# Kernel optimization log

Hardware: AMD Instinct MI355X
Metric: run time of the kernel (lower is better)

The kernel has to match this reference:

```python
import jax, jax.numpy as jnp
import numpy as np

N = 100000        # nodes
E = 1_600_000     # edges (avg degree 16)
F_IN = 128        # in_channels
HID = 64          # hidden_channels (per-head)
H1 = 4            # heads layer 1
G = 128           # number of graphs
NEG_SLOPE = 0.2   # PyG GATConv default leaky_relu slope


def setup_inputs() -> dict:
    key = jax.random.key(0)
    ks = jax.random.split(key, 12)
    x = jax.random.normal(ks[0], (N, F_IN), dtype=jnp.float32)
    edge_index = jax.random.randint(ks[1], (2, E), 0, N, dtype=jnp.int64)
    batch = jnp.sort(jax.random.randint(ks[2], (N,), 0, G, dtype=jnp.int64))
    s1 = 1.0 / np.sqrt(F_IN)
    s2 = 1.0 / np.sqrt(H1 * HID)
    # layer 1: in=F_IN, out=H1*HID (PyG lin has no bias; separate bias after concat)
    w1 = jax.random.normal(ks[3], (H1 * HID, F_IN), dtype=jnp.float32) * s1
    a_src1 = jax.random.normal(ks[4], (H1, HID), dtype=jnp.float32) * s1
    a_dst1 = jax.random.normal(ks[5], (H1, HID), dtype=jnp.float32) * s1
    b1 = jnp.zeros((H1 * HID,), dtype=jnp.float32)
    # layer 2: in=H1*HID, out=HID, heads=1
    w2 = jax.random.normal(ks[6], (1 * HID, H1 * HID), dtype=jnp.float32) * s2
    a_src2 = jax.random.normal(ks[7], (1, HID), dtype=jnp.float32) * s2
    a_dst2 = jax.random.normal(ks[8], (1, HID), dtype=jnp.float32) * s2
    b2 = jnp.zeros((HID,), dtype=jnp.float32)
    return {"x": x, "w1": w1, "a_src1": a_src1, "a_dst1": a_dst1, "b1": b1,
            "w2": w2, "a_src2": a_src2, "a_dst2": a_dst2, "b2": b2,
            "edge_index": edge_index, "batch": batch}


def _segment_softmax(alpha, seg, n):
    # numerically-stable softmax of alpha [E,H] grouped by seg (dst node)
    m = jax.ops.segment_max(alpha, seg, num_segments=n)
    m = jnp.where(jnp.isfinite(m), m, 0.0)  # empty segments -> 0
    a = jnp.exp(alpha - m[seg])
    s = jax.ops.segment_sum(a, seg, num_segments=n)
    return a / (s[seg] + 1e-16)


def _gat_conv(x, w, a_src, a_dst, bias, src, dst, n, heads, ch):
    h = (x @ w.T).reshape(n, heads, ch)          # [N,H,C]
    alpha_src = jnp.sum(h * a_src[None], axis=-1)  # [N,H]
    alpha_dst = jnp.sum(h * a_dst[None], axis=-1)  # [N,H]
    e = jax.nn.leaky_relu(alpha_src[src] + alpha_dst[dst], NEG_SLOPE)  # [E,H]
    att = _segment_softmax(e, dst, n)             # [E,H]
    msg = h[src] * att[:, :, None]                # [E,H,C]
    out = jax.ops.segment_sum(msg, dst, num_segments=n)  # [N,H,C]
    return out.reshape(n, heads * ch) + bias


def reference(x, w1, a_src1, a_dst1, b1, w2, a_src2, a_dst2, b2, edge_index, batch):
    src, dst = edge_index[0], edge_index[1]
    h = jax.nn.relu(_gat_conv(x, w1, a_src1, a_dst1, b1, src, dst, N, H1, HID))
    h = jax.nn.relu(_gat_conv(h, w2, a_src2, a_dst2, b2, src, dst, N, 1, HID))
    # global_mean_pool over graph ids
    sums = jax.ops.segment_sum(h, batch, num_segments=G)            # [G,HID]
    cnt = jax.ops.segment_sum(jnp.ones((N,), h.dtype), batch, num_segments=G)
    return sums / jnp.maximum(cnt, 1.0)[:, None]
```

## Files before the change

kernel.cpp:

```cpp
#include <hip/hip_runtime.h>
#include <math.h>
#include <type_traits>

#define NNODES 100000
#define NEDGES 1600000
#define NGRAPH 128
#define NBKT 391
#define CAP 1536
#define EPB 2048

typedef _Float16 f16x4 __attribute__((ext_vector_type(4)));
typedef _Float16 f16x8 __attribute__((ext_vector_type(8)));
typedef float f32x4 __attribute__((ext_vector_type(4)));

__global__ void convert_w(const float* __restrict__ w1, const float* __restrict__ w2,
                          const float* __restrict__ as1c, const float* __restrict__ ad1c,
                          const float* __restrict__ as2c, const float* __restrict__ ad2c,
                          _Float16* __restrict__ w1h, _Float16* __restrict__ w2h,
                          _Float16* __restrict__ va1, _Float16* __restrict__ va2) {
  const int b = blockIdx.x, tid = threadIdx.x;
  if (b < 8) {
    if (tid >= 128) return;
    int h = b & 3;
    const float* coef = (b >= 4) ? ad1c : as1c;
    float s = 0.f;
    for (int c = 0; c < 64; ++c) s = fmaf(w1[(size_t)(h * 64 + c) * 128 + tid], coef[h * 64 + c], s);
    va1[b * 128 + tid] = (_Float16)s;
  } else if (b < 10) {
    int r = b - 8;
    const float* coef = r ? ad2c : as2c;
    float s = 0.f;
    for (int c = 0; c < 64; ++c) s = fmaf(w2[(size_t)c * 256 + tid], coef[c], s);
    va2[r * 256 + tid] = (_Float16)s;
  } else if (b < 138) {
    int i = (b - 10) * 256 + tid;
    w1h[i] = (_Float16)w1[i];
  } else {
    int i = (b - 138) * 256 + tid;
    w2h[i] = (_Float16)w2[i];
  }
}

template <int K, int N, typename AT>
__global__ __launch_bounds__(256) void gemm_mfma(const AT* __restrict__ A,
    const _Float16* __restrict__ Bh, const _Float16* __restrict__ VA,
    _Float16* __restrict__ C, int M, float* __restrict__ asrc, float* __restrict__ adst) {
  constexpr int H = N / 64;
  constexpr int KS = K / 32, NT = N / 16;
  const int lane = threadIdx.x & 63, wid = threadIdx.x >> 6;
  const int lr = lane & 15;
  const int lk = (lane >> 4) * 8;
  const int row = blockIdx.x * 64 + wid * 16 + lr;

  f16x8 a[KS];
  if (row < M) {
    const AT* arow = A + (size_t)row * K;
#pragma unroll
    for (int ks = 0; ks < KS; ++ks) {
      if constexpr (std::is_same<AT, float>::value) {
        float4 v0 = *(const float4*)&arow[ks * 32 + lk];
        float4 v1 = *(const float4*)&arow[ks * 32 + lk + 4];
        f16x8 t;
        t[0] = (_Float16)v0.x; t[1] = (_Float16)v0.y; t[2] = (_Float16)v0.z; t[3] = (_Float16)v0.w;
        t[4] = (_Float16)v1.x; t[5] = (_Float16)v1.y; t[6] = (_Float16)v1.z; t[7] = (_Float16)v1.w;
        a[ks] = t;
      } else {
        a[ks] = *(const f16x8*)&arow[ks * 32 + lk];
      }
    }
  } else {
#pragma unroll
    for (int ks = 0; ks < KS; ++ks) a[ks] = (f16x8){};
  }

  f32x4 accv = (f32x4){0.f, 0.f, 0.f, 0.f};
  {
    const _Float16* vrow = VA + (size_t)lr * K;
#pragma unroll
    for (int ks = 0; ks < KS; ++ks) {
      f16x8 b = *(const f16x8*)&vrow[ks * 32 + lk];
      accv = __builtin_amdgcn_mfma_f32_16x16x32_f16(a[ks], b, accv, 0, 0, 0);
    }
  }

  f32x4 acc[NT];
#pragma unroll
  for (int nt = 0; nt < NT; ++nt) acc[nt] = (f32x4){0.f, 0.f, 0.f, 0.f};
#pragma unroll
  for (int nt = 0; nt < NT; ++nt) {
    const _Float16* brow = Bh + (size_t)(nt * 16 + lr) * K;
#pragma unroll
    for (int ks = 0; ks < KS; ++ks) {
      f16x8 b = *(const f16x8*)&brow[ks * 32 + lk];
      acc[nt] = __builtin_amdgcn_mfma_f32_16x16x32_f16(a[ks], b, acc[nt], 0, 0, 0);
    }
  }

  int row0 = blockIdx.x * 64 + wid * 16 + (lane >> 4) * 4;
#pragma unroll
  for (int r = 0; r < 4; ++r) {
    int orow = row0 + r;
    if (orow >= M) continue;
#pragma unroll
    for (int nt = 0; nt < NT; ++nt)
      C[(size_t)orow * N + nt * 16 + lr] = (_Float16)acc[nt][r];
    if (lr < H) asrc[orow * H + lr] = accv[r];
    else if (lr < 2 * H) adst[orow * H + lr - H] = accv[r];
  }
}

__global__ __launch_bounds__(256) void bucketA(const int* __restrict__ srcv,
    const int* __restrict__ dstv, int2* __restrict__ part, int* __restrict__ gcur,
    int e_count) {
  __shared__ int hist[NBKT];
  __shared__ int base_[NBKT];
  __shared__ int lofs[NBKT];
  const int tid = threadIdx.x;
  const int P = blockIdx.x & 7;
  for (int i = tid; i < NBKT; i += 256) { hist[i] = 0; lofs[i] = 0; }
  __syncthreads();
  const int e0 = blockIdx.x * EPB;
  const int e1 = min(e0 + EPB, e_count);
  for (int e = e0 + tid; e < e1; e += 256) atomicAdd(&hist[dstv[e] >> 8], 1);
  __syncthreads();
  for (int i = tid; i < NBKT; i += 256) {
    int c = hist[i];
    base_[i] = c ? atomicAdd(&gcur[(P * NBKT + i) * 16], c) : 0;
  }
  __syncthreads();
  for (int e = e0 + tid; e < e1; e += 256) {
    int d = dstv[e];
    int b = d >> 8;
    int l = atomicAdd(&lofs[b], 1);
    part[(size_t)(P * NBKT + b) * CAP + base_[b] + l] = make_int2(srcv[e], d);
  }
}

__global__ __launch_bounds__(256) void bucketB1(const int2* __restrict__ part,
    const int* __restrict__ gcur, int* __restrict__ deg, int n) {
  __shared__ int cnt[256];
  const int b = blockIdx.x;
  const int tid = threadIdx.x;
  cnt[tid] = 0;
  __syncthreads();
  for (int P = 0; P < 8; ++P) {
    int cn = gcur[(P * NBKT + b) * 16];
    const int2* seg = part + (size_t)(P * NBKT + b) * CAP;
    for (int i = tid; i < cn; i += 256) atomicAdd(&cnt[seg[i].y & 255], 1);
  }
  __syncthreads();
  int node = (b << 8) + tid;
  if (node < n) deg[node] = cnt[tid];
}

__global__ __launch_bounds__(256) void bucketB2(const int2* __restrict__ part,
    const int* __restrict__ gcur, const int* __restrict__ offsets,
    int* __restrict__ esrc, int n) {
  __shared__ int lcur[256];
  const int b = blockIdx.x;
  const int tid = threadIdx.x;
  int node = (b << 8) + tid;
  lcur[tid] = (node < n) ? offsets[node] : 0;
  __syncthreads();
  for (int P = 0; P < 8; ++P) {
    int cn = gcur[(P * NBKT + b) * 16];
    const int2* seg = part + (size_t)(P * NBKT + b) * CAP;
    for (int i = tid; i < cn; i += 256) {
      int2 e = seg[i];
      int slot = atomicAdd(&lcur[e.y & 255], 1);
      esrc[slot] = e.x;
    }
  }
}

__global__ __launch_bounds__(1024) void scan1(const int* __restrict__ deg, int* __restrict__ inc,
                                              int* __restrict__ bsum, int n) {
  __shared__ int sm[1024];
  int i = blockIdx.x * 1024 + threadIdx.x;
  sm[threadIdx.x] = (i < n) ? deg[i] : 0;
  __syncthreads();
  for (int o = 1; o < 1024; o <<= 1) {
    int t = (threadIdx.x >= o) ? sm[threadIdx.x - o] : 0;
    __syncthreads();
    sm[threadIdx.x] += t;
    __syncthreads();
  }
  if (i < n) inc[i] = sm[threadIdx.x];
  if (threadIdx.x == 1023) bsum[blockIdx.x] = sm[1023];
}

__global__ void scan2(const int* __restrict__ bsum, int* __restrict__ boff, int nb) {
  __shared__ int sm[128];
  int t = threadIdx.x;
  int own = (t < nb) ? bsum[t] : 0;
  sm[t] = own;
  __syncthreads();
  for (int o = 1; o < 128; o <<= 1) {
    int u = (t >= o) ? sm[t - o] : 0;
    __syncthreads();
    sm[t] += u;
    __syncthreads();
  }
  if (t < nb) boff[t] = sm[t] - own;
}

__global__ void scan3(const int* __restrict__ inc, const int* __restrict__ deg,
                      const int* __restrict__ boff, int* __restrict__ offsets,
                      int n, int e_count) {
  int i = blockIdx.x * blockDim.x + threadIdx.x;
  if (i < n) offsets[i] = inc[i] - deg[i] + boff[i >> 10];
  if (i == 0) offsets[n] = e_count;
}

__global__ __launch_bounds__(256) void agg1_kernel(const _Float16* __restrict__ hmat,
    const float* __restrict__ asrc, const float* __restrict__ adst,
    const int* __restrict__ offsets, const int* __restrict__ esrc,
    const float* __restrict__ bias, _Float16* __restrict__ outv) {
  const int lane = threadIdx.x & 63, wid = threadIdx.x >> 6;
  const int node = blockIdx.x * 4 + wid;
  if (node >= NNODES) return;
  const int h = lane >> 4;
  const int start = offsets[node];
  const int end = offsets[node + 1];
  const float adn = adst[node * 4 + h];
  const _Float16* hbase = hmat + lane * 4;
  float acc[4] = {0.f, 0.f, 0.f, 0.f};
  float s = 0.f;
  int j = start;
  for (; j + 8 <= end; j += 8) {
    int sv[8];
#pragma unroll
    for (int t = 0; t < 8; ++t) sv[t] = esrc[j + t];
    f16x4 vv[8];
#pragma unroll
    for (int t = 0; t < 8; ++t) vv[t] = *(const f16x4*)&hbase[(size_t)sv[t] * 256];
    _Float16 ph[8];
#pragma unroll
    for (int t = 0; t < 8; ++t) {
      float v = asrc[sv[t] * 4 + h] + adn;
      v = (v > 0.f) ? v : 0.2f * v;
      float p = __expf(v);
      s += p;
      ph[t] = (_Float16)p;
    }
#pragma unroll
    for (int t = 0; t < 8; ++t)
#pragma unroll
      for (int k = 0; k < 4; ++k)
        acc[k] = fmaf((float)vv[t][k], (float)ph[t], acc[k]);
  }
  for (; j < end; ++j) {
    int sv = esrc[j];
    f16x4 vv = *(const f16x4*)&hbase[(size_t)sv * 256];
    float v = asrc[sv * 4 + h] + adn;
    v = (v > 0.f) ? v : 0.2f * v;
    float p = __expf(v);
    s += p;
    _Float16 phs = (_Float16)p;
#pragma unroll
    for (int k = 0; k < 4; ++k) acc[k] = fmaf((float)vv[k], (float)phs, acc[k]);
  }
  float inv = 1.f / (s + 1e-16f);
  f16x4 ho;
#pragma unroll
  for (int k = 0; k < 4; ++k)
    ho[k] = (_Float16)fmaxf(fmaf(acc[k], inv, bias[lane * 4 + k]), 0.f);
  *(f16x4*)&outv[(size_t)node * 256 + lane * 4] = ho;
}

__global__ __launch_bounds__(256) void agg2_kernel(const _Float16* __restrict__ hmat,
    const float* __restrict__ asrc, const float* __restrict__ adst,
    const int* __restrict__ offsets, const int* __restrict__ esrc,
    const float* __restrict__ bias, float* __restrict__ outv) {
  const int lane = threadIdx.x & 63, wid = threadIdx.x >> 6;
  const int g = lane >> 4, q = lane & 15;
  const int node = blockIdx.x * 16 + wid * 4 + g;
  if (node >= NNODES) return;
  const int start = offsets[node];
  const int end = offsets[node + 1];
  const float adn = adst[node];
  const _Float16* hbase = hmat + q * 4;
  float acc[4] = {0.f, 0.f, 0.f, 0.f};
  float s = 0.f;
  int j = start;
  for (; j + 4 <= end; j += 4) {
    int sv[4];
#pragma unroll
    for (int t = 0; t < 4; ++t) sv[t] = esrc[j + t];
    f16x4 v[4];
#pragma unroll
    for (int t = 0; t < 4; ++t) v[t] = *(const f16x4*)&hbase[(size_t)sv[t] * 64];
#pragma unroll
    for (int t = 0; t < 4; ++t) {
      float x = asrc[sv[t]] + adn;
      x = (x > 0.f) ? x : 0.2f * x;
      float p = __expf(x);
      s += p;
      _Float16 phs = (_Float16)p;
#pragma unroll
      for (int k = 0; k < 4; ++k) acc[k] = fmaf((float)v[t][k], (float)phs, acc[k]);
    }
  }
  for (; j < end; ++j) {
    int sv = esrc[j];
    f16x4 v = *(const f16x4*)&hbase[(size_t)sv * 64];
    float x = asrc[sv] + adn;
    x = (x > 0.f) ? x : 0.2f * x;
    float p = __expf(x);
    s += p;
    _Float16 phs = (_Float16)p;
#pragma unroll
    for (int k = 0; k < 4; ++k) acc[k] = fmaf((float)v[k], (float)phs, acc[k]);
  }
  float inv = 1.f / (s + 1e-16f);
  float4 o;
  o.x = fmaxf(fmaf(acc[0], inv, bias[q * 4 + 0]), 0.f);
  o.y = fmaxf(fmaf(acc[1], inv, bias[q * 4 + 1]), 0.f);
  o.z = fmaxf(fmaf(acc[2], inv, bias[q * 4 + 2]), 0.f);
  o.w = fmaxf(fmaf(acc[3], inv, bias[q * 4 + 3]), 0.f);
  *(float4*)&outv[(size_t)node * 64 + q * 4] = o;
}

__global__ __launch_bounds__(256) void pool_kernel(const float* __restrict__ g2,
    const int* __restrict__ batch, float* __restrict__ out, int n) {
  const int gid = blockIdx.x;
  const int lane = threadIdx.x & 63, w = threadIdx.x >> 6;
  int lo = 0, hi = n;
  while (lo < hi) { int mid = (lo + hi) >> 1; if (batch[mid] < gid) lo = mid + 1; else hi = mid; }
  int lb = lo;
  hi = n;
  while (lo < hi) { int mid = (lo + hi) >> 1; if (batch[mid] < gid + 1) lo = mid + 1; else hi = mid; }
  int ub = lo;
  float acc = 0.f;
  for (int i = lb + w; i < ub; i += 4) acc += g2[(size_t)i * 64 + lane];
  __shared__ float red[4][64];
  red[w][lane] = acc;
  __syncthreads();
  if (threadIdx.x < 64) {
    float sum = (red[0][lane] + red[1][lane]) + (red[2][lane] + red[3][lane]);
    float cnt = fmaxf((float)(ub - lb), 1.f);
    out[gid * 64 + lane] = sum / cnt;
  }
}

extern "C" void kernel_launch(void* const* d_in, const int* in_sizes, int n_in,
                              void* d_out, int out_size, void* d_ws, size_t ws_size,
                              hipStream_t stream) {
  const float* x      = (const float*)d_in[0];
  const float* w1     = (const float*)d_in[1];
  const float* a_src1 = (const float*)d_in[2];
  const float* a_dst1 = (const float*)d_in[3];
  const float* b1     = (const float*)d_in[4];
  const float* w2     = (const float*)d_in[5];
  const float* a_src2 = (const float*)d_in[6];
  const float* a_dst2 = (const float*)d_in[7];
  const float* b2     = (const float*)d_in[8];
  const int*   src    = (const int*)d_in[9];
  const int*   dst    = src + NEDGES;
  const int*   batch  = (const int*)d_in[10];
  float* out = (float*)d_out;

  const int N = NNODES, E = NEDGES;
  const int NB = (N + 1023) / 1024;

  char* wsb = (char*)d_ws;
  size_t off = 0;
  auto alloc = [&](size_t bytes) {
    void* p = wsb + off;
    off = (off + bytes + 255) & ~(size_t)255;
    return p;
  };
  _Float16* h1h = (_Float16*)alloc((size_t)N * 256 * 2);
  _Float16* g1h = (_Float16*)alloc((size_t)N * 256 * 2);
  _Float16* h2h = (_Float16*)alloc((size_t)N * 64 * 2);
  float* g2     = (float*)alloc((size_t)N * 64 * 4);
  float* as1    = (float*)alloc((size_t)N * 4 * 4);
  float* ad1    = (float*)alloc((size_t)N * 4 * 4);
  float* as2    = (float*)alloc((size_t)N * 4);
  float* ad2    = (float*)alloc((size_t)N * 4);
  int* deg      = (int*)alloc((size_t)N * 4);
  int* inc      = (int*)alloc((size_t)N * 4);
  int* bsum     = (int*)alloc((size_t)NB * 4);
  int* boff     = (int*)alloc((size_t)NB * 4);
  int* offsets  = (int*)alloc((size_t)(N + 1) * 4);
  int* esrc     = (int*)alloc((size_t)E * 4);
  int2* part    = (int2*)alloc((size_t)8 * NBKT * CAP * 8);
  int* gcur     = (int*)alloc((size_t)8 * NBKT * 16 * 4);
  _Float16* w1h = (_Float16*)alloc((size_t)256 * 128 * 2);
  _Float16* w2h = (_Float16*)alloc((size_t)64 * 256 * 2);
  _Float16* va1 = (_Float16*)alloc((size_t)16 * 128 * 2);
  _Float16* va2 = (_Float16*)alloc((size_t)16 * 256 * 2);

  hipMemsetAsync(va1, 0, (size_t)16 * 128 * 2, stream);
  hipMemsetAsync(va2, 0, (size_t)16 * 256 * 2, stream);
  convert_w<<<202, 256, 0, stream>>>(w1, w2, a_src1, a_dst1, a_src2, a_dst2,
                                     w1h, w2h, va1, va2);

  hipMemsetAsync(gcur, 0, (size_t)8 * NBKT * 16 * 4, stream);
  bucketA<<<(E + EPB - 1) / EPB, 256, 0, stream>>>(src, dst, part, gcur, E);
  bucketB1<<<NBKT, 256, 0, stream>>>(part, gcur, deg, N);
  scan1<<<NB, 1024, 0, stream>>>(deg, inc, bsum, N);
  scan2<<<1, 128, 0, stream>>>(bsum, boff, NB);
  scan3<<<(N + 255) / 256, 256, 0, stream>>>(inc, deg, boff, offsets, N, E);
  bucketB2<<<NBKT, 256, 0, stream>>>(part, gcur, offsets, esrc, N);

  gemm_mfma<128, 256, float><<<(N + 63) / 64, 256, 0, stream>>>(
      x, w1h, va1, h1h, N, as1, ad1);
  agg1_kernel<<<(N + 3) / 4, 256, 0, stream>>>(h1h, as1, ad1, offsets, esrc, b1, g1h);

  gemm_mfma<256, 64, _Float16><<<(N + 63) / 64, 256, 0, stream>>>(
      g1h, w2h, va2, h2h, N, as2, ad2);
  agg2_kernel<<<(N + 15) / 16, 256, 0, stream>>>(h2h, as2, ad2, offsets, esrc, b2, g2);

  pool_kernel<<<NGRAPH, 256, 0, stream>>>(g2, batch, out, N);
}
```

Before: 411.2 us.

## Prefetch next B tile in MFMA GEMM and split agg1 into four launches

The GEMM now loads all attention-vector B fragments before issuing their MFMAs, and double-buffers the weight fragments, fetching the next N-tile's B rows while the current tile's MFMAs run. This is meant to hide global load latency behind matrix work, at the cost of more registers. Separately, the layer-1 aggregation is split into four sequential launches over node quarters, which adds launch overhead with no obvious benefit. The split looks like an experiment, possibly aimed at cache locality.

```diff
diff --git a/kernel.cpp b/kernel.cpp
--- a/kernel.cpp
+++ b/kernel.cpp
@@ -76,24 +76,36 @@
   f32x4 accv = (f32x4){0.f, 0.f, 0.f, 0.f};
   {
     const _Float16* vrow = VA + (size_t)lr * K;
-#pragma unroll
-    for (int ks = 0; ks < KS; ++ks) {
-      f16x8 b = *(const f16x8*)&vrow[ks * 32 + lk];
-      accv = __builtin_amdgcn_mfma_f32_16x16x32_f16(a[ks], b, accv, 0, 0, 0);
+    f16x8 bv[KS];
+#pragma unroll
+    for (int ks = 0; ks < KS; ++ks) bv[ks] = *(const f16x8*)&vrow[ks * 32 + lk];
+#pragma unroll
+    for (int ks = 0; ks < KS; ++ks)
+      accv = __builtin_amdgcn_mfma_f32_16x16x32_f16(a[ks], bv[ks], accv, 0, 0, 0);
+  }
+
+  f32x4 acc[NT];
+#pragma unroll
+  for (int nt = 0; nt < NT; ++nt) acc[nt] = (f32x4){0.f, 0.f, 0.f, 0.f};
+
+  f16x8 bc[KS], bn[KS];
+  {
+    const _Float16* brow = Bh + (size_t)lr * K;
+#pragma unroll
+    for (int ks = 0; ks < KS; ++ks) bc[ks] = *(const f16x8*)&brow[ks * 32 + lk];
+  }
+#pragma unroll
+  for (int nt = 0; nt < NT; ++nt) {
+    if (nt + 1 < NT) {
+      const _Float16* brow = Bh + (size_t)((nt + 1) * 16 + lr) * K;
+#pragma unroll
+      for (int ks = 0; ks < KS; ++ks) bn[ks] = *(const f16x8*)&brow[ks * 32 + lk];
     }
-  }
-
-  f32x4 acc[NT];
-#pragma unroll
-  for (int nt = 0; nt < NT; ++nt) acc[nt] = (f32x4){0.f, 0.f, 0.f, 0.f};
-#pragma unroll
-  for (int nt = 0; nt < NT; ++nt) {
-    const _Float16* brow = Bh + (size_t)(nt * 16 + lr) * K;
-#pragma unroll
-    for (int ks = 0; ks < KS; ++ks) {
-      f16x8 b = *(const f16x8*)&brow[ks * 32 + lk];
-      acc[nt] = __builtin_amdgcn_mfma_f32_16x16x32_f16(a[ks], b, acc[nt], 0, 0, 0);
-    }
+#pragma unroll
+    for (int ks = 0; ks < KS; ++ks)
+      acc[nt] = __builtin_amdgcn_mfma_f32_16x16x32_f16(a[ks], bc[ks], acc[nt], 0, 0, 0);
+#pragma unroll
+    for (int ks = 0; ks < KS; ++ks) bc[ks] = bn[ks];
   }
 
   int row0 = blockIdx.x * 64 + wid * 16 + (lane >> 4) * 4;
@@ -215,10 +227,10 @@
 __global__ __launch_bounds__(256) void agg1_kernel(const _Float16* __restrict__ hmat,
     const float* __restrict__ asrc, const float* __restrict__ adst,
     const int* __restrict__ offsets, const int* __restrict__ esrc,
-    const float* __restrict__ bias, _Float16* __restrict__ outv) {
+    const float* __restrict__ bias, _Float16* __restrict__ outv, int node0, int node_end) {
   const int lane = threadIdx.x & 63, wid = threadIdx.x >> 6;
-  const int node = blockIdx.x * 4 + wid;
-  if (node >= NNODES) return;
+  const int node = node0 + blockIdx.x * 4 + wid;
+  if (node >= node_end) return;
   const int h = lane >> 4;
   const int start = offsets[node];
   const int end = offsets[node + 1];
@@ -406,7 +418,10 @@
 
   gemm_mfma<128, 256, float><<<(N + 63) / 64, 256, 0, stream>>>(
       x, w1h, va1, h1h, N, as1, ad1);
-  agg1_kernel<<<(N + 3) / 4, 256, 0, stream>>>(h1h, as1, ad1, offsets, esrc, b1, g1h);
+  agg1_kernel<<<6250, 256, 0, stream>>>(h1h, as1, ad1, offsets, esrc, b1, g1h, 0, 25000);
+  agg1_kernel<<<6250, 256, 0, stream>>>(h1h, as1, ad1, offsets, esrc, b1, g1h, 25000, 50000);
+  agg1_kernel<<<6250, 256, 0, stream>>>(h1h, as1, ad1, offsets, esrc, b1, g1h, 50000, 75000);
+  agg1_kernel<<<6250, 256, 0, stream>>>(h1h, as1, ad1, offsets, esrc, b1, g1h, 75000, 100000);
 
   gemm_mfma<256, 64, _Float16><<<(N + 63) / 64, 256, 0, stream>>>(
       g1h, w2h, va2, h2h, N, as2, ad2);
```

Result: slower. 432.2 us (+5.1%).
